# Kernel tuning notes

Hardware: AMD Instinct MI355X
Metric: run time of the kernel (lower is better)

Reference implementation:

```python
import jax, jax.numpy as jnp
import numpy as np

DIM = 1024
NUM_HEADS = 16
HEAD_DIM = DIM // NUM_HEADS
SCALE = HEAD_DIM ** -0.5


def setup_inputs() -> dict:
    key = jax.random.key(0)
    ks = jax.random.split(key, 5)
    x = jax.random.normal(ks[0], (4, 1024, DIM), dtype=jnp.float32)
    w_qkv = jax.random.normal(ks[1], (DIM, 3 * DIM), dtype=jnp.float32) * (DIM ** -0.5)
    b_qkv = jnp.zeros((3 * DIM,), dtype=jnp.float32)
    w_proj = jax.random.normal(ks[2], (DIM, DIM), dtype=jnp.float32) * (DIM ** -0.5)
    b_proj = jnp.zeros((DIM,), dtype=jnp.float32)
    return {"x": x, "w_qkv": w_qkv, "b_qkv": b_qkv, "w_proj": w_proj, "b_proj": b_proj}


def reference(x, w_qkv, b_qkv, w_proj, b_proj):
    B, N, C = x.shape
    qkv = x @ w_qkv + b_qkv                                  # [B, N, 3C]
    qkv = qkv.reshape(B, N, 3, NUM_HEADS, HEAD_DIM)
    qkv = jnp.transpose(qkv, (2, 0, 3, 1, 4))                # [3, B, H, N, d]
    q, k, v = qkv[0] * SCALE, qkv[1], qkv[2]
    # attn scores in float32 (clamp to finfo range is a no-op after the cast)
    attn = jnp.einsum('bhnd,bhmd->bhnm', q, k).astype(jnp.float32)
    f32 = jnp.finfo(jnp.float32)
    attn = jnp.clip(attn, f32.min, f32.max)
    attn = jax.nn.softmax(attn, axis=-1)
    out = jnp.einsum('bhnm,bhmd->bhnd', attn, v)             # [B, H, N, d]
    out = jnp.transpose(out, (0, 2, 1, 3)).reshape(B, N, C)
    return out @ w_proj + b_proj
```

## Files before the change

### kernel.cpp

```cpp
#include <hip/hip_runtime.h>


typedef _Float16 half8 __attribute__((ext_vector_type(8)));
typedef _Float16 half4v __attribute__((ext_vector_type(4)));
typedef __fp16 fp16x2 __attribute__((ext_vector_type(2)));
typedef float floatx4 __attribute__((ext_vector_type(4)));

#define MFMA16(a, b, c) __builtin_amdgcn_mfma_f32_16x16x32_f16((a), (b), (c), 0, 0, 0)

static constexpr int DIM = 1024;
static constexpr int BATCH = 4;
static constexpr int SEQ = 1024;
static constexpr int NH = 16;
static constexpr int HD = 64;
static constexpr float SCALE = 0.125f;

__device__ static inline void gld16(_Float16* lds, const _Float16* g) {
    __builtin_amdgcn_global_load_lds(
        (const __attribute__((address_space(1))) void*)g,
        (__attribute__((address_space(3))) void*)lds, 16, 0, 0);
}

__global__ __launch_bounds__(256) void prep(const float* __restrict__ x,
                                            _Float16* __restrict__ xh,
                                            const float* __restrict__ wqkv,
                                            _Float16* __restrict__ wqkvT,
                                            const float* __restrict__ wproj,
                                            _Float16* __restrict__ wprojT) {
    __shared__ float tile[32][33];
    const int bid = blockIdx.x;
    const int tid = threadIdx.x;
    if (bid < 4096) {
        int i = (bid * 256 + tid) * 4;
        float4 v = *reinterpret_cast<const float4*>(x + i);
        half4v h;
        h[0] = (_Float16)v.x; h[1] = (_Float16)v.y;
        h[2] = (_Float16)v.z; h[3] = (_Float16)v.w;
        const int m = i >> 10, k = i & 1023;
        *reinterpret_cast<half4v*>(
            &xh[((size_t)(k >> 5) * 4096 + m) * 32 + (k & 31)]) = h;
        return;
    }
    const float* in;
    _Float16* out;
    int C, NN, bx, by;
    if (bid < 7168) {
        int b = bid - 4096;
        in = wqkv; out = wqkvT; C = 3072; NN = 3072;
        bx = b % 96; by = b / 96;
    } else {
        int b = bid - 7168;
        in = wproj; out = wprojT; C = 1024; NN = 1024;
        bx = b & 31; by = b >> 5;
    }
    const int c0 = bx * 32, r0 = by * 32;
    const int tx = tid & 31, ty = tid >> 5;
#pragma unroll
    for (int j = 0; j < 32; j += 8)
        tile[ty + j][tx] = in[(size_t)(r0 + ty + j) * C + (c0 + tx)];
    __syncthreads();
#pragma unroll
    for (int j = 0; j < 32; j += 8)
        out[((size_t)(r0 >> 5) * NN + (c0 + ty + j)) * 32 + tx] =
            (_Float16)tile[tx][ty + j];
}

template <int MODE>
__global__ __launch_bounds__(256) void gemm_bt(const _Float16* __restrict__ A,
                                               const _Float16* __restrict__ Bt,
                                               const float* __restrict__ bias, int N,
                                               float* __restrict__ outF,
                                               _Float16* __restrict__ qbuf,
                                               _Float16* __restrict__ kbuf,
                                               _Float16* __restrict__ vtbuf) {
    constexpr int NT = 32;
    __shared__ _Float16 S[4][2][4096];

    const int tid = threadIdx.x;
    const int wid = tid >> 6;
    const int lane = tid & 63;
    const int g = lane >> 4;
    const int ln = lane & 15;
    const int wr = wid >> 1, wc = wid & 1;
    const int m0 = blockIdx.y * 128;
    const int n0 = blockIdx.x * 128;
    const size_t PA = (size_t)4096 * 32;
    const size_t PB = (size_t)N * 32;
    const int lsw = (lane >> 2) * 32 + (((lane & 3) ^ ((lane >> 3) & 3)) * 8);
    const int gsw = (g ^ ((ln >> 1) & 3)) * 8;
    const _Float16* ga = A + ((size_t)(m0 + wr * 64)) * 32 + lsw;
    const _Float16* gb = Bt + ((size_t)(n0 + wc * 64)) * 32 + lsw;
    _Float16* Sw = &S[wid][0][0];

    floatx4 acc[4][4];
#pragma unroll
    for (int i = 0; i < 4; ++i)
#pragma unroll
        for (int j = 0; j < 4; ++j) acc[i][j] = (floatx4){0.f, 0.f, 0.f, 0.f};

#pragma unroll
    for (int c = 0; c < 4; ++c) {
        gld16(Sw + c * 512, ga + c * 512);
        gld16(Sw + 2048 + c * 512, gb + c * 512);
    }

    for (int kt = 0; kt < NT; ++kt) {
        const int cur = kt & 1;
        if (kt < NT - 1) {
            const size_t ka = (size_t)(kt + 1) * PA;
            const size_t kb = (size_t)(kt + 1) * PB;
            _Float16* Sn = Sw + (cur ^ 1) * 4096;
#pragma unroll
            for (int c = 0; c < 4; ++c) {
                gld16(Sn + c * 512, ga + ka + c * 512);
                gld16(Sn + 2048 + c * 512, gb + kb + c * 512);
            }
            asm volatile("s_waitcnt vmcnt(8)" ::: "memory");
        } else {
            asm volatile("s_waitcnt vmcnt(0)" ::: "memory");
        }
        const _Float16* Sc = Sw + cur * 4096;

        half8 af[4], bf[4];
#pragma unroll
        for (int i = 0; i < 4; ++i)
            af[i] = *reinterpret_cast<const half8*>(&Sc[(i * 16 + ln) * 32 + gsw]);
#pragma unroll
        for (int j = 0; j < 4; ++j)
            bf[j] = *reinterpret_cast<const half8*>(&Sc[2048 + (j * 16 + ln) * 32 + gsw]);
#pragma unroll
        for (int i = 0; i < 4; ++i)
#pragma unroll
            for (int j = 0; j < 4; ++j) acc[i][j] = MFMA16(af[i], bf[j], acc[i][j]);
    }

#pragma unroll
    for (int i = 0; i < 4; ++i) {
#pragma unroll
        for (int j = 0; j < 4; ++j) {
            const int n = n0 + wc * 64 + j * 16 + ln;
            const float bn = bias[n];
            const int mrow = m0 + wr * 64 + i * 16 + g * 4;
            if (MODE == 0) {
                const int which = n >> 10;
                const int rem = n & 1023;
                const int h = rem >> 6;
                const int dd = rem & 63;
                const int b = mrow >> 10, tok = mrow & 1023;
                const int bh = b * NH + h;
                if (which == 2) {
                    half4v pk;
#pragma unroll
                    for (int r = 0; r < 4; ++r) pk[r] = (_Float16)(acc[i][j][r] + bn);
                    *reinterpret_cast<half4v*>(
                        &vtbuf[((size_t)(bh * 32 + (tok >> 5)) * 64 + dd) * 32 +
                               (tok & 31)]) = pk;
                } else if (which == 1) {
#pragma unroll
                    for (int r = 0; r < 4; ++r)
                        kbuf[((size_t)(bh * 2 + (dd >> 5)) * SEQ + tok + r) * 32 +
                             (dd & 31)] = (_Float16)(acc[i][j][r] + bn);
                } else {
#pragma unroll
                    for (int r = 0; r < 4; ++r)
                        qbuf[(size_t)((bh << 10) + tok + r) * HD + dd] =
                            (_Float16)((acc[i][j][r] + bn) * SCALE);
                }
            } else {
#pragma unroll
                for (int r = 0; r < 4; ++r)
                    outF[(size_t)(mrow + r) * N + n] = acc[i][j][r] + bn;
            }
        }
    }
}

__global__ __launch_bounds__(256, 4) void flash_attn(const _Float16* __restrict__ qbuf,
                                                     const _Float16* __restrict__ kbuf,
                                                     const _Float16* __restrict__ vtbuf,
                                                     _Float16* __restrict__ attn_out) {
    __shared__ _Float16 Klds[2 * 4096];
    __shared__ _Float16 Vlds[2 * 4096];

    const int tid = threadIdx.x;
    const int wid = tid >> 6;
    const int lane = tid & 63;
    const int g = lane >> 4;
    const int ln = lane & 15;
    const int bh = blockIdx.x;
    const int qbase = blockIdx.y * 64 + wid * 16;
    const _Float16* qg = qbuf + ((size_t)bh << 10) * HD;
    const _Float16* kg = kbuf + (size_t)bh * (2 * SEQ * 32);
    const _Float16* vg = vtbuf + (size_t)bh * (32 * 64 * 32);

    const int woff = wid * 512;
    const int lsw = (lane >> 2) * 32 + (((lane & 3) ^ ((lane >> 3) & 3)) * 8);
    const int gsw = (g ^ ((ln >> 1) & 3)) * 8;
    const int sl0 = ((lane >> 4) & 1) * 32 + ln;
    const bool hi32 = (lane & 32) != 0;

    half8 qf[2];
#pragma unroll
    for (int f = 0; f < 2; ++f)
        qf[f] = *reinterpret_cast<const half8*>(
            qg + (size_t)(qbase + ln) * HD + f * 32 + g * 8);

    floatx4 o[4];
#pragma unroll
    for (int t = 0; t < 4; ++t) o[t] = (floatx4){0.f, 0.f, 0.f, 0.f};
    float l_lane = 0.f;

    constexpr int NT = SEQ / 64;
#pragma unroll
    for (int f = 0; f < 2; ++f) {
        gld16(&Klds[f * 2048 + woff], kg + (size_t)f * (SEQ * 32) + woff + lsw);
        gld16(&Vlds[f * 2048 + woff], vg + (size_t)f * 2048 + woff + lsw);
    }

    for (int kt = 0; kt < NT; ++kt) {
        asm volatile("s_waitcnt vmcnt(0)" ::: "memory");
        asm volatile("s_barrier" ::: "memory");
        const int cur = kt & 1;
        if (kt < NT - 1) {
            const int nb = cur ^ 1;
#pragma unroll
            for (int f = 0; f < 2; ++f) {
                gld16(&Klds[nb * 4096 + f * 2048 + woff],
                      kg + (size_t)f * (SEQ * 32) + (kt + 1) * 2048 + woff + lsw);
                gld16(&Vlds[nb * 4096 + f * 2048 + woff],
                      vg + (size_t)(2 * (kt + 1) + f) * 2048 + woff + lsw);
            }
        }
        const _Float16* Kb = &Klds[cur * 4096];
        const _Float16* Vb = &Vlds[cur * 4096];

        half8 kf[4][2], vf[4][2];
#pragma unroll
        for (int c = 0; c < 4; ++c)
#pragma unroll
            for (int f = 0; f < 2; ++f) {
                kf[c][f] = *reinterpret_cast<const half8*>(
                    &Kb[f * 2048 + (c * 16 + ln) * 32 + gsw]);
                vf[c][f] = *reinterpret_cast<const half8*>(
                    &Vb[f * 2048 + (c * 16 + ln) * 32 + gsw]);
            }

        floatx4 st[4];
#pragma unroll
        for (int c = 0; c < 4; ++c) {
            floatx4 z = (floatx4){0.f, 0.f, 0.f, 0.f};
            z = MFMA16(kf[c][0], qf[0], z);
            z = MFMA16(kf[c][1], qf[1], z);
            st[c] = z;
        }

        int pk[4][2];
#pragma unroll
        for (int c = 0; c < 4; ++c) {
            float p0 = __expf(st[c][0]);
            float p1 = __expf(st[c][1]);
            float p2 = __expf(st[c][2]);
            float p3 = __expf(st[c][3]);
            l_lane += (p0 + p1) + (p2 + p3);
            union { fp16x2 h; int i; } u0, u1;
            u0.h = __builtin_amdgcn_cvt_pkrtz(p0, p1);
            u1.h = __builtin_amdgcn_cvt_pkrtz(p2, p3);
            pk[c][0] = u0.i;
            pk[c][1] = u1.i;
        }

#pragma unroll
        for (int H = 0; H < 2; ++H) {
            int a0 = __shfl(pk[2 * H][0], sl0), b0 = __shfl(pk[2 * H + 1][0], sl0);
            int a1 = __shfl(pk[2 * H][1], sl0), b1 = __shfl(pk[2 * H + 1][1], sl0);
            int a2 = __shfl(pk[2 * H][0], sl0 + 16), b2 = __shfl(pk[2 * H + 1][0], sl0 + 16);
            int a3 = __shfl(pk[2 * H][1], sl0 + 16), b3 = __shfl(pk[2 * H + 1][1], sl0 + 16);
            union { int i[4]; half8 h; } ua;
            ua.i[0] = hi32 ? b0 : a0;
            ua.i[1] = hi32 ? b1 : a1;
            ua.i[2] = hi32 ? b2 : a2;
            ua.i[3] = hi32 ? b3 : a3;
#pragma unroll
            for (int t = 0; t < 4; ++t) o[t] = MFMA16(ua.h, vf[t][H], o[t]);
        }
    }

    l_lane += __shfl_xor(l_lane, 16);
    l_lane += __shfl_xor(l_lane, 32);

    const int b = bh >> 4, h = bh & 15;
#pragma unroll
    for (int r = 0; r < 4; ++r) {
        const float inv = 1.0f / __shfl(l_lane, g * 4 + r);
        const int tok = qbase + g * 4 + r;
#pragma unroll
        for (int t = 0; t < 4; ++t)
            attn_out[((size_t)(h * 2 + (t >> 1)) * 4096 + (b * SEQ + tok)) * 32 +
                     (t & 1) * 16 + ln] = (_Float16)(o[t][r] * inv);
    }
}

extern "C" void kernel_launch(void* const* d_in, const int* in_sizes, int n_in,
                              void* d_out, int out_size, void* d_ws, size_t ws_size,
                              hipStream_t stream) {
    const float* x = (const float*)d_in[0];
    const float* wqkv = (const float*)d_in[1];
    const float* bqkv = (const float*)d_in[2];
    const float* wproj = (const float*)d_in[3];
    const float* bproj = (const float*)d_in[4];
    float* out = (float*)d_out;

    char* ws = (char*)d_ws;
    _Float16* xh     = (_Float16*)(ws);
    _Float16* wqkvT  = (_Float16*)(ws + (8ull << 20));
    _Float16* qbuf   = (_Float16*)(ws + (14ull << 20));
    _Float16* kbuf   = (_Float16*)(ws + (22ull << 20));
    _Float16* vtbuf  = (_Float16*)(ws + (30ull << 20));
    _Float16* wprojT = (_Float16*)(ws + (38ull << 20));
    _Float16* attn   = xh;

    prep<<<8192, 256, 0, stream>>>(x, xh, wqkv, wqkvT, wproj, wprojT);
    gemm_bt<0><<<dim3(24, 32), 256, 0, stream>>>(xh, wqkvT, bqkv, 3 * DIM, nullptr,
                                                 qbuf, kbuf, vtbuf);
    flash_attn<<<dim3(BATCH * NH, SEQ / 64), 256, 0, stream>>>(qbuf, kbuf, vtbuf, attn);
    gemm_bt<1><<<dim3(8, 32), 256, 0, stream>>>(attn, wprojT, bproj, DIM, out,
                                                nullptr, nullptr, nullptr);
}
```

Before: 176.8 us.

## Load GEMM B operand and attention K tiles directly to registers

In the tiled GEMM, the A tile now goes into a block-shared double buffer, with each warp loading a quarter. The B fragments are loaded straight from global memory into registers and prefetched one k-step ahead, which shrinks LDS use. In flash attention, K fragments are likewise read directly from global into registers and prefetched for the next tile, so only V stays staged in LDS. The 4-wave occupancy hint is dropped. The aim is to cut LDS traffic and footprint, at the cost of a block-wide barrier in the GEMM and global-load latency exposed on the register path.

After: 203.4 us. +15.0%, slower.

```diff
diff --git a/kernel.cpp b/kernel.cpp
--- a/kernel.cpp
+++ b/kernel.cpp
@@ -74,7 +74,7 @@
                                                _Float16* __restrict__ kbuf,
                                                _Float16* __restrict__ vtbuf) {
     constexpr int NT = 32;
-    __shared__ _Float16 S[4][2][4096];
+    __shared__ _Float16 Ah[2][4096];
 
     const int tid = threadIdx.x;
     const int wid = tid >> 6;
@@ -88,9 +88,8 @@
     const size_t PB = (size_t)N * 32;
     const int lsw = (lane >> 2) * 32 + (((lane & 3) ^ ((lane >> 3) & 3)) * 8);
     const int gsw = (g ^ ((ln >> 1) & 3)) * 8;
-    const _Float16* ga = A + ((size_t)(m0 + wr * 64)) * 32 + lsw;
-    const _Float16* gb = Bt + ((size_t)(n0 + wc * 64)) * 32 + lsw;
-    _Float16* Sw = &S[wid][0][0];
+    const _Float16* ga = A + (size_t)(m0 + wid * 32) * 32 + lsw;
+    const _Float16* gbw = Bt + (size_t)(n0 + wc * 64) * 32;
 
     floatx4 acc[4][4];
 #pragma unroll
@@ -98,40 +97,40 @@
 #pragma unroll
         for (int j = 0; j < 4; ++j) acc[i][j] = (floatx4){0.f, 0.f, 0.f, 0.f};
 
-#pragma unroll
-    for (int c = 0; c < 4; ++c) {
-        gld16(Sw + c * 512, ga + c * 512);
-        gld16(Sw + 2048 + c * 512, gb + c * 512);
-    }
+    gld16(&Ah[0][wid * 1024], ga);
+    gld16(&Ah[0][wid * 1024 + 512], ga + 512);
+    half8 bf[4];
+#pragma unroll
+    for (int j = 0; j < 4; ++j)
+        bf[j] = *reinterpret_cast<const half8*>(gbw + (j * 16 + ln) * 32 + g * 8);
 
     for (int kt = 0; kt < NT; ++kt) {
         const int cur = kt & 1;
+        asm volatile("s_waitcnt vmcnt(0)" ::: "memory");
+        asm volatile("s_barrier" ::: "memory");
         if (kt < NT - 1) {
             const size_t ka = (size_t)(kt + 1) * PA;
+            gld16(&Ah[cur ^ 1][wid * 1024], ga + ka);
+            gld16(&Ah[cur ^ 1][wid * 1024 + 512], ga + ka + 512);
+        }
+
+        half8 af[4];
+#pragma unroll
+        for (int i = 0; i < 4; ++i)
+            af[i] = *reinterpret_cast<const half8*>(
+                &Ah[cur][(wr * 64 + i * 16 + ln) * 32 + gsw]);
+#pragma unroll
+        for (int i = 0; i < 4; ++i)
+#pragma unroll
+            for (int j = 0; j < 4; ++j) acc[i][j] = MFMA16(af[i], bf[j], acc[i][j]);
+
+        if (kt < NT - 1) {
             const size_t kb = (size_t)(kt + 1) * PB;
-            _Float16* Sn = Sw + (cur ^ 1) * 4096;
-#pragma unroll
-            for (int c = 0; c < 4; ++c) {
-                gld16(Sn + c * 512, ga + ka + c * 512);
-                gld16(Sn + 2048 + c * 512, gb + kb + c * 512);
-            }
-            asm volatile("s_waitcnt vmcnt(8)" ::: "memory");
-        } else {
-            asm volatile("s_waitcnt vmcnt(0)" ::: "memory");
-        }
-        const _Float16* Sc = Sw + cur * 4096;
-
-        half8 af[4], bf[4];
-#pragma unroll
-        for (int i = 0; i < 4; ++i)
-            af[i] = *reinterpret_cast<const half8*>(&Sc[(i * 16 + ln) * 32 + gsw]);
-#pragma unroll
-        for (int j = 0; j < 4; ++j)
-            bf[j] = *reinterpret_cast<const half8*>(&Sc[2048 + (j * 16 + ln) * 32 + gsw]);
-#pragma unroll
-        for (int i = 0; i < 4; ++i)
-#pragma unroll
-            for (int j = 0; j < 4; ++j) acc[i][j] = MFMA16(af[i], bf[j], acc[i][j]);
+#pragma unroll
+            for (int j = 0; j < 4; ++j)
+                bf[j] = *reinterpret_cast<const half8*>(
+                    gbw + kb + (j * 16 + ln) * 32 + g * 8);
+        }
     }
 
 #pragma unroll
@@ -175,12 +174,11 @@
     }
 }
 
-__global__ __launch_bounds__(256, 4) void flash_attn(const _Float16* __restrict__ qbuf,
-                                                     const _Float16* __restrict__ kbuf,
-                                                     const _Float16* __restrict__ vtbuf,
-                                                     _Float16* __restrict__ attn_out) {
-    __shared__ _Float16 Klds[2 * 4096];
-    __shared__ _Float16 Vlds[2 * 4096];
+__global__ __launch_bounds__(256) void flash_attn(const _Float16* __restrict__ qbuf,
+                                                  const _Float16* __restrict__ kbuf,
+                                                  const _Float16* __restrict__ vtbuf,
+                                                  _Float16* __restrict__ attn_out) {
+    __shared__ _Float16 Vlds[2][4096];
 
     const int tid = threadIdx.x;
     const int wid = tid >> 6;
@@ -212,38 +210,34 @@
 
     constexpr int NT = SEQ / 64;
 #pragma unroll
-    for (int f = 0; f < 2; ++f) {
-        gld16(&Klds[f * 2048 + woff], kg + (size_t)f * (SEQ * 32) + woff + lsw);
-        gld16(&Vlds[f * 2048 + woff], vg + (size_t)f * 2048 + woff + lsw);
-    }
+    for (int f = 0; f < 2; ++f)
+        gld16(&Vlds[0][f * 2048 + woff], vg + (size_t)f * 2048 + woff + lsw);
+    half8 kf[4][2];
+#pragma unroll
+    for (int c = 0; c < 4; ++c)
+#pragma unroll
+        for (int f = 0; f < 2; ++f)
+            kf[c][f] = *reinterpret_cast<const half8*>(
+                kg + (size_t)f * (SEQ * 32) + (c * 16 + ln) * 32 + g * 8);
 
     for (int kt = 0; kt < NT; ++kt) {
         asm volatile("s_waitcnt vmcnt(0)" ::: "memory");
         asm volatile("s_barrier" ::: "memory");
         const int cur = kt & 1;
         if (kt < NT - 1) {
-            const int nb = cur ^ 1;
-#pragma unroll
-            for (int f = 0; f < 2; ++f) {
-                gld16(&Klds[nb * 4096 + f * 2048 + woff],
-                      kg + (size_t)f * (SEQ * 32) + (kt + 1) * 2048 + woff + lsw);
-                gld16(&Vlds[nb * 4096 + f * 2048 + woff],
+#pragma unroll
+            for (int f = 0; f < 2; ++f)
+                gld16(&Vlds[cur ^ 1][f * 2048 + woff],
                       vg + (size_t)(2 * (kt + 1) + f) * 2048 + woff + lsw);
-            }
-        }
-        const _Float16* Kb = &Klds[cur * 4096];
-        const _Float16* Vb = &Vlds[cur * 4096];
-
-        half8 kf[4][2], vf[4][2];
+        }
+
+        half8 vf[4][2];
 #pragma unroll
         for (int c = 0; c < 4; ++c)
 #pragma unroll
-            for (int f = 0; f < 2; ++f) {
-                kf[c][f] = *reinterpret_cast<const half8*>(
-                    &Kb[f * 2048 + (c * 16 + ln) * 32 + gsw]);
+            for (int f = 0; f < 2; ++f)
                 vf[c][f] = *reinterpret_cast<const half8*>(
-                    &Vb[f * 2048 + (c * 16 + ln) * 32 + gsw]);
-            }
+                    &Vlds[cur][f * 2048 + (c * 16 + ln) * 32 + gsw]);
 
         floatx4 st[4];
 #pragma unroll
@@ -252,6 +246,16 @@
             z = MFMA16(kf[c][0], qf[0], z);
             z = MFMA16(kf[c][1], qf[1], z);
             st[c] = z;
+        }
+
+        if (kt < NT - 1) {
+            const int kr1 = (kt + 1) * 64;
+#pragma unroll
+            for (int c = 0; c < 4; ++c)
+#pragma unroll
+                for (int f = 0; f < 2; ++f)
+                    kf[c][f] = *reinterpret_cast<const half8*>(
+                        kg + (size_t)f * (SEQ * 32) + (kr1 + c * 16 + ln) * 32 + g * 8);
         }
 
         int pk[4][2];
```

## Shrink GEMM tile to 64x128 with block-shared LDS operands and barriers

Applied to the files above, without the earlier changes.

The GEMM drops from 128x128 to 64x128 block tiles, which doubles the grid for both projection GEMMs. A and B tiles now sit in LDS shared by the whole block, so waves reuse each other's loaded data instead of each wave staging its own 64x64 slice. Each k-step now needs a full vmcnt(0) wait plus a block barrier, which serializes loading and compute more than the old per-wave vmcnt(8) double buffer did. The aim is better CU occupancy on the small proj GEMM (256 to 512 blocks) and fewer redundant global loads, at the cost of synchronization and lower MFMA work per wave.

Measured after the change: 187.7 us. 1.06x slower.

```diff
diff --git a/kernel.cpp b/kernel.cpp
--- a/kernel.cpp
+++ b/kernel.cpp
@@ -74,7 +74,8 @@
                                                _Float16* __restrict__ kbuf,
                                                _Float16* __restrict__ vtbuf) {
     constexpr int NT = 32;
-    __shared__ _Float16 S[4][2][4096];
+    __shared__ _Float16 Ah[2][2048];
+    __shared__ _Float16 Bh[2][4096];
 
     const int tid = threadIdx.x;
     const int wid = tid >> 6;
@@ -82,65 +83,59 @@
     const int g = lane >> 4;
     const int ln = lane & 15;
     const int wr = wid >> 1, wc = wid & 1;
-    const int m0 = blockIdx.y * 128;
+    const int m0 = blockIdx.y * 64;
     const int n0 = blockIdx.x * 128;
     const size_t PA = (size_t)4096 * 32;
     const size_t PB = (size_t)N * 32;
     const int lsw = (lane >> 2) * 32 + (((lane & 3) ^ ((lane >> 3) & 3)) * 8);
     const int gsw = (g ^ ((ln >> 1) & 3)) * 8;
-    const _Float16* ga = A + ((size_t)(m0 + wr * 64)) * 32 + lsw;
-    const _Float16* gb = Bt + ((size_t)(n0 + wc * 64)) * 32 + lsw;
-    _Float16* Sw = &S[wid][0][0];
-
-    floatx4 acc[4][4];
-#pragma unroll
-    for (int i = 0; i < 4; ++i)
+    const _Float16* ga = A + (size_t)(m0 + wid * 16) * 32 + lsw;
+    const _Float16* gb = Bt + (size_t)(n0 + wid * 32) * 32 + lsw;
+
+    floatx4 acc[2][4];
+#pragma unroll
+    for (int i = 0; i < 2; ++i)
 #pragma unroll
         for (int j = 0; j < 4; ++j) acc[i][j] = (floatx4){0.f, 0.f, 0.f, 0.f};
 
-#pragma unroll
-    for (int c = 0; c < 4; ++c) {
-        gld16(Sw + c * 512, ga + c * 512);
-        gld16(Sw + 2048 + c * 512, gb + c * 512);
-    }
+    gld16(&Ah[0][wid * 512], ga);
+    gld16(&Bh[0][wid * 1024], gb);
+    gld16(&Bh[0][wid * 1024 + 512], gb + 512);
 
     for (int kt = 0; kt < NT; ++kt) {
         const int cur = kt & 1;
+        asm volatile("s_waitcnt vmcnt(0)" ::: "memory");
+        asm volatile("s_barrier" ::: "memory");
         if (kt < NT - 1) {
             const size_t ka = (size_t)(kt + 1) * PA;
             const size_t kb = (size_t)(kt + 1) * PB;
-            _Float16* Sn = Sw + (cur ^ 1) * 4096;
-#pragma unroll
-            for (int c = 0; c < 4; ++c) {
-                gld16(Sn + c * 512, ga + ka + c * 512);
-                gld16(Sn + 2048 + c * 512, gb + kb + c * 512);
-            }
-            asm volatile("s_waitcnt vmcnt(8)" ::: "memory");
-        } else {
-            asm volatile("s_waitcnt vmcnt(0)" ::: "memory");
-        }
-        const _Float16* Sc = Sw + cur * 4096;
-
-        half8 af[4], bf[4];
-#pragma unroll
-        for (int i = 0; i < 4; ++i)
-            af[i] = *reinterpret_cast<const half8*>(&Sc[(i * 16 + ln) * 32 + gsw]);
+            gld16(&Ah[cur ^ 1][wid * 512], ga + ka);
+            gld16(&Bh[cur ^ 1][wid * 1024], gb + kb);
+            gld16(&Bh[cur ^ 1][wid * 1024 + 512], gb + kb + 512);
+        }
+
+        half8 af[2], bf[4];
+#pragma unroll
+        for (int i = 0; i < 2; ++i)
+            af[i] = *reinterpret_cast<const half8*>(
+                &Ah[cur][(wr * 32 + i * 16 + ln) * 32 + gsw]);
 #pragma unroll
         for (int j = 0; j < 4; ++j)
-            bf[j] = *reinterpret_cast<const half8*>(&Sc[2048 + (j * 16 + ln) * 32 + gsw]);
-#pragma unroll
-        for (int i = 0; i < 4; ++i)
+            bf[j] = *reinterpret_cast<const half8*>(
+                &Bh[cur][(wc * 64 + j * 16 + ln) * 32 + gsw]);
+#pragma unroll
+        for (int i = 0; i < 2; ++i)
 #pragma unroll
             for (int j = 0; j < 4; ++j) acc[i][j] = MFMA16(af[i], bf[j], acc[i][j]);
     }
 
 #pragma unroll
-    for (int i = 0; i < 4; ++i) {
+    for (int i = 0; i < 2; ++i) {
 #pragma unroll
         for (int j = 0; j < 4; ++j) {
             const int n = n0 + wc * 64 + j * 16 + ln;
             const float bn = bias[n];
-            const int mrow = m0 + wr * 64 + i * 16 + g * 4;
+            const int mrow = m0 + wr * 32 + i * 16 + g * 4;
             if (MODE == 0) {
                 const int which = n >> 10;
                 const int rem = n & 1023;
@@ -320,9 +315,9 @@
     _Float16* attn   = xh;
 
     prep<<<8192, 256, 0, stream>>>(x, xh, wqkv, wqkvT, wproj, wprojT);
-    gemm_bt<0><<<dim3(24, 32), 256, 0, stream>>>(xh, wqkvT, bqkv, 3 * DIM, nullptr,
+    gemm_bt<0><<<dim3(24, 64), 256, 0, stream>>>(xh, wqkvT, bqkv, 3 * DIM, nullptr,
                                                  qbuf, kbuf, vtbuf);
     flash_attn<<<dim3(BATCH * NH, SEQ / 64), 256, 0, stream>>>(qbuf, kbuf, vtbuf, attn);
-    gemm_bt<1><<<dim3(8, 32), 256, 0, stream>>>(attn, wprojT, bproj, DIM, out,
+    gemm_bt<1><<<dim3(8, 64), 256, 0, stream>>>(attn, wprojT, bproj, DIM, out,
                                                 nullptr, nullptr, nullptr);
 }
```
